# Kernel tuning notes

Hardware: AMD Instinct MI355X
Metric: run time of the kernel (lower is better)

## Reference

```python
import jax, jax.numpy as jnp
import numpy as np
from jax import lax

B, S, PH, N = 4, 512, 4096, 16384
D, G, H, L, FF, GS = 1024, 128, 8, 4, 4096, 32
HD = D // H


def setup_inputs() -> dict:
    key = jax.random.key(0)
    ks = list(jax.random.split(key, 16))
    r = lambda k, sh: jax.random.normal(k, sh, jnp.float32) * 0.02
    return {
        'last_hidden': jax.random.normal(ks[0], (B, S, PH), jnp.float32),
        'current_pointcloud': jax.random.normal(ks[1], (B, N, 3), jnp.float32),
        'fp_w': r(ks[2], (D, PH)), 'fp_b': jnp.zeros((D,), jnp.float32),
        'sp_w': r(ks[3], (G * D, D)), 'sp_b': jnp.zeros((G * D,), jnp.float32),
        'pos_embed': r(ks[4], (1, G, D)),
        'ln1_w': jnp.ones((L, D), jnp.float32), 'ln1_b': jnp.zeros((L, D), jnp.float32),
        'in_w': r(ks[5], (L, 3 * D, D)), 'in_b': jnp.zeros((L, 3 * D), jnp.float32),
        'out_w': r(ks[6], (L, D, D)), 'out_b': jnp.zeros((L, D), jnp.float32),
        'ln2_w': jnp.ones((L, D), jnp.float32), 'ln2_b': jnp.zeros((L, D), jnp.float32),
        'mlp_w1': r(ks[7], (L, FF, D)), 'mlp_b1': jnp.zeros((L, FF), jnp.float32),
        'mlp_w2': r(ks[8], (L, D, FF)), 'mlp_b2': jnp.zeros((L, D), jnp.float32),
        'c1_w': r(ks[9], (D, D)), 'c1_b': jnp.zeros((D,), jnp.float32),
        'bn_g': jnp.ones((D,), jnp.float32), 'bn_beta': jnp.zeros((D,), jnp.float32),
        'bn_m': jnp.zeros((D,), jnp.float32), 'bn_v': jnp.ones((D,), jnp.float32),
        'c2_w': r(ks[10], (3 * GS, D)), 'c2_b': jnp.zeros((3 * GS,), jnp.float32),
    }


def _ln(x, w, b):
    m = jnp.mean(x, -1, keepdims=True)
    v = jnp.mean(jnp.square(x - m), -1, keepdims=True)
    return (x - m) * lax.rsqrt(v + 1e-5) * w + b


def _fps(xyz, num_samples):
    # iterative farthest point sampling; deterministic start index 0
    Bb, Nn, _ = xyz.shape
    dist0 = jnp.full((Bb, Nn), 1e10, xyz.dtype)
    far0 = jnp.zeros((Bb,), jnp.int32)

    def step(carry, _):
        dist, far = carry
        centroid = jnp.take_along_axis(xyz, far[:, None, None], axis=1)  # [B,1,3]
        d = jnp.sum(jnp.square(xyz - centroid), -1)                      # [B,N]
        dist = jnp.minimum(dist, d)
        return (dist, jnp.argmax(dist, -1).astype(jnp.int32)), far

    _, cents = lax.scan(step, (dist0, far0), None, length=num_samples)
    cents = cents.T  # [B, num_samples]
    return jnp.take_along_axis(xyz, cents[:, :, None], axis=1)  # [B,num_samples,3]


def reference(last_hidden, current_pointcloud, fp_w, fp_b, sp_w, sp_b, pos_embed,
              ln1_w, ln1_b, in_w, in_b, out_w, out_b, ln2_w, ln2_b,
              mlp_w1, mlp_b1, mlp_w2, mlp_b2,
              c1_w, c1_b, bn_g, bn_beta, bn_m, bn_v, c2_w, c2_b):
    bsz = last_hidden.shape[0]
    agg = jnp.mean(last_hidden @ fp_w.T + fp_b, axis=1)          # [B,D]
    x = (agg @ sp_w.T + sp_b).reshape(bsz, G, D)                 # [B,G,D]
    centers = _fps(current_pointcloud, G)                        # [B,G,3]
    scale = 1.0 / np.sqrt(HD).astype(np.float32)

    def block(x, p):
        l1w, l1b, iw, ib, ow, ob, l2w, l2b, w1, b1, w2, b2 = p
        xn = _ln(x + pos_embed, l1w, l1b)
        qkv = xn @ iw.T + ib                                     # [B,G,3D]
        q, k, v = jnp.split(qkv, 3, axis=-1)
        hsp = lambda t: t.reshape(bsz, G, H, HD).transpose(0, 2, 1, 3)
        q, k, v = hsp(q), hsp(k), hsp(v)
        a = jax.nn.softmax(jnp.einsum('bhqd,bhkd->bhqk', q, k) * scale, axis=-1)
        o = jnp.einsum('bhqk,bhkd->bhqd', a, v).transpose(0, 2, 1, 3).reshape(bsz, G, D)
        x = x + o @ ow.T + ob
        h = jax.nn.gelu(_ln(x, l2w, l2b) @ w1.T + b1, approximate=False)
        return x + h @ w2.T + b2, None

    x, _ = lax.scan(block, x, (ln1_w, ln1_b, in_w, in_b, out_w, out_b,
                               ln2_w, ln2_b, mlp_w1, mlp_b1, mlp_w2, mlp_b2))

    # future_predictor: 1x1 conv == per-token linear; BN in eval mode
    h = x @ c1_w.T + c1_b
    h = jax.nn.relu((h - bn_m) * lax.rsqrt(bn_v + 1e-5) * bn_g + bn_beta)
    deltas = (h @ c2_w.T + c2_b).reshape(bsz * G, GS, 3)
    pred = deltas + centers.reshape(bsz * G, 1, 3)
    return pred.reshape(bsz, G * GS, 3)
```

## Files before the change

kernel.cpp:

```cpp
#include <hip/hip_runtime.h>
#include <hip/hip_bf16.h>
#include <math.h>


typedef __bf16 bf16x8_t __attribute__((ext_vector_type(8)));
typedef float  f32x4_t  __attribute__((ext_vector_type(4)));

__device__ __forceinline__ float wredsum(float v){
#pragma unroll
  for (int o = 32; o; o >>= 1) v += __shfl_down(v, o, 64);
  return v;
}

__device__ __forceinline__ bf16x8_t pack8(float4 a, float4 b){
  bf16x8_t v;
  v[0]=(__bf16)a.x; v[1]=(__bf16)a.y; v[2]=(__bf16)a.z; v[3]=(__bf16)a.w;
  v[4]=(__bf16)b.x; v[5]=(__bf16)b.y; v[6]=(__bf16)b.z; v[7]=(__bf16)b.w;
  return v;
}

__device__ __forceinline__ void gload16(const void* g, void* l){
  __builtin_amdgcn_global_load_lds((const __attribute__((address_space(1))) unsigned int*)g,
                                   (__attribute__((address_space(3))) unsigned int*)l, 16, 0, 0);
}

__global__ __launch_bounds__(1024) void fused_front(
  const float* __restrict__ pc, float* __restrict__ centers,
  const float* __restrict__ agg, const float* __restrict__ spw,
  const float* __restrict__ spb, float* __restrict__ x,
  const float* __restrict__ inw, const float* __restrict__ outw,
  const float* __restrict__ w1, const float* __restrict__ w2,
  const float* __restrict__ c1w, __bf16* __restrict__ wbf)
{
  const int bid = blockIdx.x;
  const int tid = threadIdx.x;
  if (bid < 4){
    const int b = bid;
    const int lane = tid & 63;
    const float* base = pc + (size_t)b * 16384 * 3;
    float px[16], py[16], pz[16], dist[16];
    {
      union { float4 v4[12]; float f[48]; } u;
      const float4* src = (const float4*)(base + tid * 48);
#pragma unroll
      for (int q = 0; q < 12; ++q) u.v4[q] = src[q];
#pragma unroll
      for (int j = 0; j < 16; ++j){
        px[j] = u.f[j*3]; py[j] = u.f[j*3+1]; pz[j] = u.f[j*3+2];
        dist[j] = 1e10f;
      }
    }
    __shared__ unsigned long long keyslot[128];
    for (int i = tid; i < 128; i += 1024) keyslot[i] = 0ULL;
    __syncthreads();
    float cx = base[0], cy = base[1], cz = base[2];
    for (int t = 0; t < 128; ++t){
      if (tid == 0){
        centers[(b*128+t)*3+0] = cx;
        centers[(b*128+t)*3+1] = cy;
        centers[(b*128+t)*3+2] = cz;
      }
      if (t == 127) break;
      float bmax = -1.0f; int bidx = 0;
#pragma unroll
      for (int j = 0; j < 16; ++j){
        float dx = __fsub_rn(px[j], cx);
        float dy = __fsub_rn(py[j], cy);
        float dz = __fsub_rn(pz[j], cz);
        float d  = __fadd_rn(__fadd_rn(__fmul_rn(dx,dx), __fmul_rn(dy,dy)), __fmul_rn(dz,dz));
        float nd = fminf(dist[j], d);
        dist[j] = nd;
        if (nd > bmax){ bmax = nd; bidx = tid*16 + j; }
      }
      unsigned long long key = ((unsigned long long)__float_as_uint(bmax) << 32)
                             | (unsigned long long)(0xFFFFFFFFu - (unsigned)bidx);
#pragma unroll
      for (int o = 32; o; o >>= 1){
        unsigned long long ok = __shfl_down(key, o, 64);
        if (ok > key) key = ok;
      }
      if (lane == 0) atomicMax(&keyslot[t], key);
      __syncthreads();
      const unsigned long long gk = keyslot[t];
      const unsigned gidx = 0xFFFFFFFFu - (unsigned)(gk & 0xFFFFFFFFu);
      const float* cp = base + (size_t)gidx*3;
      cx = cp[0]; cy = cp[1]; cz = cp[2];
    }
  } else if (bid < 1028){
    __shared__ float ag[4096];
    for (int i = tid; i < 4096; i += 1024) ag[i] = agg[i];
    __syncthreads();
    const int wv = tid >> 6, lane = tid & 63;
    const int rbase = ((bid - 4)*16 + wv)*8;
    for (int rr = 0; rr < 8; ++rr){
      const int row = rbase + rr;
      const float* wp = spw + (size_t)row*1024 + lane*4;
      const float4 w0 = *(const float4*)(wp      );
      const float4 wq1 = *(const float4*)(wp + 256);
      const float4 wq2 = *(const float4*)(wp + 512);
      const float4 wq3 = *(const float4*)(wp + 768);
      float acc[4];
#pragma unroll
      for (int bb = 0; bb < 4; ++bb){
        const float* gp = &ag[bb*1024 + lane*4];
        const float4 g0 = *(const float4*)(gp      );
        const float4 g1 = *(const float4*)(gp + 256);
        const float4 g2 = *(const float4*)(gp + 512);
        const float4 g3 = *(const float4*)(gp + 768);
        acc[bb] = w0.x*g0.x + w0.y*g0.y + w0.z*g0.z + w0.w*g0.w
                + wq1.x*g1.x + wq1.y*g1.y + wq1.z*g1.z + wq1.w*g1.w
                + wq2.x*g2.x + wq2.y*g2.y + wq2.z*g2.z + wq2.w*g2.w
                + wq3.x*g3.x + wq3.y*g3.y + wq3.z*g3.z + wq3.w*g3.w;
      }
      float a0 = wredsum(acc[0]);
      float a1 = wredsum(acc[1]);
      float a2 = wredsum(acc[2]);
      float a3 = wredsum(acc[3]);
      if (lane == 0){
        const float bias = spb[row];
        x[(size_t)0*131072 + row] = a0 + bias;
        x[(size_t)1*131072 + row] = a1 + bias;
        x[(size_t)2*131072 + row] = a2 + bias;
        x[(size_t)3*131072 + row] = a3 + bias;
      }
    }
  } else {
    const size_t t = (size_t)(bid - 1028)*1024 + tid;
    const size_t i = t*8;
    const float* src;
    if (i < 50331648){
      const size_t l = i / 12582912, r = i - l*12582912;
      if (r < 3145728)       src = inw  + l*3145728 + r;
      else if (r < 4194304)  src = outw + l*1048576 + (r-3145728);
      else if (r < 8388608)  src = w1   + l*4194304 + (r-4194304);
      else                   src = w2   + l*4194304 + (r-8388608);
    } else src = c1w + (i - 50331648);
    float4 a = *(const float4*)src, bq = *(const float4*)(src+4);
    *(bf16x8_t*)(wbf + i) = pack8(a, bq);
  }
}

__global__ __launch_bounds__(256) void partial_kernel(const float* __restrict__ lh,
                                                      float* __restrict__ part){
  const int ph = blockIdx.x*256 + threadIdx.x;
  const int sc = blockIdx.y, b = blockIdx.z;
  const float* p = lh + ((size_t)b*512 + sc*64)*4096 + ph;
  float s0=0,s1=0,s2=0,s3=0;
  for (int j = 0; j < 64; j += 4){
    s0 += p[(size_t)(j+0)*4096];
    s1 += p[(size_t)(j+1)*4096];
    s2 += p[(size_t)(j+2)*4096];
    s3 += p[(size_t)(j+3)*4096];
  }
  part[(size_t)(b*8+sc)*4096 + ph] = (s0+s1)+(s2+s3);
}

__global__ __launch_bounds__(256) void combine_kernel(const float* __restrict__ part,
                                                      float* __restrict__ mlh){
  const int i = blockIdx.x*256 + threadIdx.x;
  const int b = i >> 12, ph = i & 4095;
  float s = 0;
#pragma unroll
  for (int sc = 0; sc < 8; ++sc) s += part[(size_t)(b*8+sc)*4096 + ph];
  mlh[i] = s * (1.0f/512.0f);
}

__global__ __launch_bounds__(256) void agg_kernel(const float* __restrict__ mlh,
                                                  const float* __restrict__ fpw,
                                                  const float* __restrict__ fpb,
                                                  float* __restrict__ agg){
  const int o = blockIdx.x*4 + (threadIdx.x>>6);
  const int lane = threadIdx.x & 63;
  const int b = o >> 10, d = o & 1023;
  const float* mp = mlh + b*4096;
  const float* wp = fpw + (size_t)d*4096;
  float s = 0;
#pragma unroll 4
  for (int j = 0; j < 64; ++j){
    int ph = lane + j*64;
    s += mp[ph] * wp[ph];
  }
  s = wredsum(s);
  if (lane == 0) agg[o] = s + fpb[d];
}

__global__ __launch_bounds__(256) void ln_kernel(const float* __restrict__ x,
                                                 const float* __restrict__ pos,
                                                 const float* __restrict__ w,
                                                 const float* __restrict__ bb,
                                                 __bf16* __restrict__ out){
  const int tok = blockIdx.x, g = tok & 127, t = threadIdx.x;
  const int lane = t & 63, wv = t >> 6;
  const float* xr = x + (size_t)tok*1024;
  float v[4];
#pragma unroll
  for (int j = 0; j < 4; ++j){
    int d = t + j*256;
    float val = xr[d];
    if (pos) val += pos[g*1024 + d];
    v[j] = val;
  }
  __shared__ float r1[4], r2[4];
  float s = wredsum(v[0]+v[1]+v[2]+v[3]);
  if (lane == 0) r1[wv] = s;
  __syncthreads();
  const float mean = (r1[0]+r1[1]+r1[2]+r1[3]) * (1.0f/1024.0f);
  float sq = 0;
#pragma unroll
  for (int j = 0; j < 4; ++j){ float d0 = v[j]-mean; sq += d0*d0; }
  sq = wredsum(sq);
  if (lane == 0) r2[wv] = sq;
  __syncthreads();
  const float var = (r2[0]+r2[1]+r2[2]+r2[3]) * (1.0f/1024.0f);
  const float rs = rsqrtf(var + 1e-5f);
#pragma unroll
  for (int j = 0; j < 4; ++j){
    int d = t + j*256;
    out[(size_t)tok*1024 + d] = (__bf16)((v[j]-mean)*rs*w[d] + bb[d]);
  }
}

__global__ __launch_bounds__(256) void gemm_sk(
  const __bf16* __restrict__ A, const __bf16* __restrict__ W,
  float* __restrict__ parts, int M, int N, int K, int kc)
{
  __shared__ __bf16 As[128*32];
  __shared__ __bf16 Ws[128*32];
  const int n0 = blockIdx.x*128, m0 = blockIdx.y*128, z = blockIdx.z;
  const int tid = threadIdx.x;
  const int lane = tid & 63, w = tid >> 6;
  const int wm = w >> 1, wn = w & 1;
  const int lr = lane & 15, g = lane >> 4;
  const int kbeg = z*kc, kend = kbeg + kc;
  f32x4_t acc[4][4] = {};
  for (int k0 = kbeg; k0 < kend; k0 += 32){
    __syncthreads();
#pragma unroll
    for (int i = 0; i < 2; ++i){
      const int c = tid + i*256;
      const int row = c >> 2, q = c & 3;
      gload16(A + (size_t)(m0+row)*K + k0 + q*8, &As[(size_t)c*8]);
      gload16(W + (size_t)(n0+row)*K + k0 + q*8, &Ws[(size_t)c*8]);
    }
    __syncthreads();
    bf16x8_t af[4], bf[4];
#pragma unroll
    for (int f = 0; f < 4; ++f){
      af[f] = *(bf16x8_t*)&As[(wm*64 + f*16 + lr)*32 + g*8];
      bf[f] = *(bf16x8_t*)&Ws[(wn*64 + f*16 + lr)*32 + g*8];
    }
#pragma unroll
    for (int i = 0; i < 4; ++i)
#pragma unroll
      for (int j = 0; j < 4; ++j)
        acc[i][j] = __builtin_amdgcn_mfma_f32_16x16x32_bf16(af[i], bf[j], acc[i][j], 0, 0, 0);
  }
  float* C = parts + (size_t)z*M*N;
#pragma unroll
  for (int i = 0; i < 4; ++i)
#pragma unroll
    for (int j = 0; j < 4; ++j)
#pragma unroll
      for (int r = 0; r < 4; ++r){
        const int row = m0 + wm*64 + i*16 + g*4 + r;
        const int col = n0 + wn*64 + j*16 + lr;
        C[(size_t)row*N + col] = acc[i][j][r];
      }
}

__global__ __launch_bounds__(256) void comb_qkv(const float* __restrict__ parts,
                                                const float* __restrict__ bias,
                                                __bf16* __restrict__ out){
  const int i = blockIdx.x*256 + threadIdx.x;
  const int col = i % 3072;
  float s = 0;
#pragma unroll
  for (int z = 0; z < 4; ++z) s += parts[(size_t)z*1572864 + i];
  out[i] = (__bf16)(s + bias[col]);
}

__global__ __launch_bounds__(256) void comb_gelu(const float* __restrict__ parts,
                                                 const float* __restrict__ bias,
                                                 __bf16* __restrict__ out){
  const int i = blockIdx.x*256 + threadIdx.x;
  const int col = i & 4095;
  float v = 0;
#pragma unroll
  for (int z = 0; z < 4; ++z) v += parts[(size_t)z*2097152 + i];
  v += bias[col];
  v = v * 0.5f * (1.0f + erff(v * 0.70710678118654752440f));
  out[i] = (__bf16)v;
}

template<int MODE>
__global__ __launch_bounds__(256) void comb_res_ln(const float* __restrict__ parts, int nsplit,
                                                   const float* __restrict__ bias,
                                                   const float* __restrict__ pos,
                                                   const float* __restrict__ lw,
                                                   const float* __restrict__ lb,
                                                   float* __restrict__ x,
                                                   __bf16* __restrict__ xn){
  const int tok = blockIdx.x, gi = tok & 127, t = threadIdx.x;
  const int lane = t & 63, wv = t >> 6;
  float v[4];
#pragma unroll
  for (int j = 0; j < 4; ++j){
    const int d = t + j*256;
    const size_t idx = (size_t)tok*1024 + d;
    float s = 0;
    for (int z = 0; z < nsplit; ++z) s += parts[(size_t)z*524288 + idx];
    float val = x[idx] + s + bias[d];
    x[idx] = val;
    v[j] = val;
  }
  if (MODE == 2){
#pragma unroll
    for (int j = 0; j < 4; ++j){
      const int d = t + j*256;
      xn[(size_t)tok*1024 + d] = (__bf16)v[j];
    }
    return;
  }
  float u[4];
#pragma unroll
  for (int j = 0; j < 4; ++j){
    const int d = t + j*256;
    u[j] = v[j] + (MODE == 1 ? pos[gi*1024 + d] : 0.0f);
  }
  __shared__ float r1[4], r2[4];
  float s1 = wredsum(u[0]+u[1]+u[2]+u[3]);
  if (lane == 0) r1[wv] = s1;
  __syncthreads();
  const float mean = (r1[0]+r1[1]+r1[2]+r1[3]) * (1.0f/1024.0f);
  float sq = 0;
#pragma unroll
  for (int j = 0; j < 4; ++j){ float d0 = u[j]-mean; sq += d0*d0; }
  sq = wredsum(sq);
  if (lane == 0) r2[wv] = sq;
  __syncthreads();
  const float var = (r2[0]+r2[1]+r2[2]+r2[3]) * (1.0f/1024.0f);
  const float rs = rsqrtf(var + 1e-5f);
#pragma unroll
  for (int j = 0; j < 4; ++j){
    const int d = t + j*256;
    xn[(size_t)tok*1024 + d] = (__bf16)((u[j]-mean)*rs*lw[d] + lb[d]);
  }
}

__global__ __launch_bounds__(256) void comb_bn(const float* __restrict__ parts, int nsplit,
                                               const float* __restrict__ bias,
                                               const float* __restrict__ bnm,
                                               const float* __restrict__ bnv,
                                               const float* __restrict__ bng,
                                               const float* __restrict__ bnb,
                                               float* __restrict__ out){
  const int i = blockIdx.x*256 + threadIdx.x;
  const int c = i & 1023;
  float s = 0;
  for (int z = 0; z < nsplit; ++z) s += parts[(size_t)z*524288 + i];
  float v = s + bias[c];
  v = (v - bnm[c]) * rsqrtf(bnv[c] + 1e-5f) * bng[c] + bnb[c];
  out[i] = fmaxf(v, 0.0f);
}

__global__ __launch_bounds__(256) void attn_fused(const __bf16* __restrict__ qkv,
                                                  __bf16* __restrict__ O){
  const int bh = blockIdx.x >> 1, half = blockIdx.x & 1;
  const int b = bh>>3, h = bh&7;
  const int tid = threadIdx.x, w = tid>>6, lane = tid&63;
  const int lr = lane&15, g = lane>>4;
  __shared__ __bf16 vt[128*128];
  __shared__ __bf16 pl[4*2048];
  {
    const int n = tid >> 1, kh = tid & 1;
    const __bf16* vbase = qkv + (size_t)(b*128)*3072 + 2048 + h*128 + n;
#pragma unroll
    for (int jb = 0; jb < 8; ++jb){
      bf16x8_t pk;
#pragma unroll
      for (int e = 0; e < 8; ++e) pk[e] = vbase[(size_t)(kh*64 + jb*8 + e)*3072];
      const int cb = kh*8 + jb;
      *(bf16x8_t*)&vt[n*128 + ((cb ^ (n&7)) * 8)] = pk;
    }
  }
  const __bf16* qbase = qkv + (size_t)(b*128)*3072 + h*128;
  const __bf16* kbase = qbase + 1024;
  const int qrow0 = half*64 + w*16;
  f32x4_t acc[8] = {};
#pragma unroll
  for (int ks = 0; ks < 4; ++ks){
    bf16x8_t aq, bk[8];
    aq = *(const bf16x8_t*)(qbase + (size_t)(qrow0 + lr)*3072 + ks*32 + g*8);
#pragma unroll
    for (int j = 0; j < 8; ++j)
      bk[j] = *(const bf16x8_t*)(kbase + (size_t)(j*16 + lr)*3072 + ks*32 + g*8);
#pragma unroll
    for (int j = 0; j < 8; ++j)
      acc[j] = __builtin_amdgcn_mfma_f32_16x16x32_bf16(aq, bk[j], acc[j], 0, 0, 0);
  }
  __syncthreads();
  const float scale = 0.088388347648318447f;
#pragma unroll
  for (int r = 0; r < 4; ++r){
    const int row = g*4 + r;
    float sv[8];
    float mx = -1e30f;
#pragma unroll
    for (int j = 0; j < 8; ++j){ sv[j] = acc[j][r]*scale; mx = fmaxf(mx, sv[j]); }
#pragma unroll
    for (int o = 1; o < 16; o <<= 1) mx = fmaxf(mx, __shfl_xor(mx, o, 64));
    float s = 0;
#pragma unroll
    for (int j = 0; j < 8; ++j){ sv[j] = expf(sv[j]-mx); s += sv[j]; }
#pragma unroll
    for (int o = 1; o < 16; o <<= 1) s += __shfl_xor(s, o, 64);
    const float inv = 1.0f/s;
#pragma unroll
    for (int j = 0; j < 8; ++j){
      const int col = j*16 + lr;
      const int slot = (col>>3) ^ (row&7);
      pl[w*2048 + row*128 + slot*8 + (lr&7)] = (__bf16)(sv[j]*inv);
    }
  }
  __syncthreads();
  f32x4_t acc2[8] = {};
#pragma unroll
  for (int ks = 0; ks < 4; ++ks){
    bf16x8_t ap, bv[8];
    {
      const int row = lr;
      const int slot = (ks*4 + g) ^ (row&7);
      ap = *(bf16x8_t*)&pl[w*2048 + row*128 + slot*8];
    }
#pragma unroll
    for (int j = 0; j < 8; ++j){
      const int rowv = j*16 + lr;
      const int cb = ks*4 + g;
      bv[j] = *(bf16x8_t*)&vt[rowv*128 + ((cb ^ (rowv&7))*8)];
    }
#pragma unroll
    for (int j = 0; j < 8; ++j)
      acc2[j] = __builtin_amdgcn_mfma_f32_16x16x32_bf16(ap, bv[j], acc2[j], 0, 0, 0);
  }
#pragma unroll
  for (int j = 0; j < 8; ++j)
#pragma unroll
    for (int r = 0; r < 4; ++r){
      const int row = qrow0 + g*4 + r;
      const int col = j*16 + lr;
      O[(size_t)(b*128+row)*1024 + h*128 + col] = (__bf16)acc2[j][r];
    }
}

__global__ __launch_bounds__(256) void c2_kernel(const float* __restrict__ hb,
                                                 const float* __restrict__ w,
                                                 const float* __restrict__ bb,
                                                 const float* __restrict__ centers,
                                                 float* __restrict__ out){
  const int o = blockIdx.x*4 + (threadIdx.x>>6);
  const int lane = threadIdx.x & 63;
  const int tok = o / 96, n = o % 96;
  const float* hp = hb + (size_t)tok*1024;
  const float* wp = w + (size_t)n*1024;
  float s = 0;
#pragma unroll 4
  for (int j = 0; j < 16; ++j){
    int k = lane + j*64;
    s += hp[k] * wp[k];
  }
  s = wredsum(s);
  if (lane == 0) out[o] = s + bb[n] + centers[tok*3 + (n % 3)];
}

extern "C" void kernel_launch(void* const* d_in, const int* in_sizes, int n_in,
                              void* d_out, int out_size, void* d_ws, size_t ws_size,
                              hipStream_t stream){
  const float* lh   = (const float*)d_in[0];
  const float* pc   = (const float*)d_in[1];
  const float* fpw  = (const float*)d_in[2];
  const float* fpb  = (const float*)d_in[3];
  const float* spw  = (const float*)d_in[4];
  const float* spb  = (const float*)d_in[5];
  const float* pos  = (const float*)d_in[6];
  const float* ln1w = (const float*)d_in[7];
  const float* ln1b = (const float*)d_in[8];
  const float* inw  = (const float*)d_in[9];
  const float* inb  = (const float*)d_in[10];
  const float* outw = (const float*)d_in[11];
  const float* outb = (const float*)d_in[12];
  const float* ln2w = (const float*)d_in[13];
  const float* ln2b = (const float*)d_in[14];
  const float* w1   = (const float*)d_in[15];
  const float* b1   = (const float*)d_in[16];
  const float* w2   = (const float*)d_in[17];
  const float* b2   = (const float*)d_in[18];
  const float* c1w  = (const float*)d_in[19];
  const float* c1b  = (const float*)d_in[20];
  const float* bng  = (const float*)d_in[21];
  const float* bnbt = (const float*)d_in[22];
  const float* bnm  = (const float*)d_in[23];
  const float* bnv  = (const float*)d_in[24];
  const float* c2w  = (const float*)d_in[25];
  const float* c2b  = (const float*)d_in[26];
  float* out = (float*)d_out;

  float* f = (float*)d_ws;
  float* parts = f;              f += 16*524288;
  float* part  = f;              f += 131072;
  float* mlh   = f;              f += 16384;
  float* agg   = f;              f += 4096;
  float* x     = f;              f += 524288;
  float* hc1   = f;              f += 524288;
  float* cent  = f;              f += 2048;
  __bf16* bfp = (__bf16*)f;
  __bf16* xn   = bfp;            bfp += 524288;
  __bf16* qkv  = bfp;            bfp += 1572864;
  __bf16* obuf = bfp;            bfp += 524288;
  __bf16* hbf  = bfp;            bfp += 2097152;
  __bf16* xbf  = bfp;            bfp += 524288;
  __bf16* wbf  = bfp;            bfp += 51380224;

  partial_kernel<<<dim3(16,8,4), 256, 0, stream>>>(lh, part);
  combine_kernel<<<64, 256, 0, stream>>>(part, mlh);
  agg_kernel<<<1024, 256, 0, stream>>>(mlh, fpw, fpb, agg);
  fused_front<<<7300, 1024, 0, stream>>>(pc, cent, agg, spw, spb, x,
                                         inw, outw, w1, w2, c1w, wbf);
  ln_kernel<<<512, 256, 0, stream>>>(x, pos, ln1w, ln1b, xn);

  for (int l = 0; l < 4; ++l){
    const __bf16* wl = wbf + (size_t)l*12582912;
    gemm_sk<<<dim3(24,4,4), 256, 0, stream>>>(xn, wl, parts, 512, 3072, 1024, 256);
    comb_qkv<<<6144, 256, 0, stream>>>(parts, inb + l*3072, qkv);
    attn_fused<<<64, 256, 0, stream>>>(qkv, obuf);
    gemm_sk<<<dim3(8,4,8), 256, 0, stream>>>(obuf, wl + 3145728, parts, 512, 1024, 1024, 128);
    comb_res_ln<0><<<512, 256, 0, stream>>>(parts, 8, outb + l*1024, nullptr,
                                            ln2w + l*1024, ln2b + l*1024, x, xn);
    gemm_sk<<<dim3(32,4,4), 256, 0, stream>>>(xn, wl + 4194304, parts, 512, 4096, 1024, 256);
    comb_gelu<<<8192, 256, 0, stream>>>(parts, b1 + l*4096, hbf);
    gemm_sk<<<dim3(8,4,16), 256, 0, stream>>>(hbf, wl + 8388608, parts, 512, 1024, 4096, 256);
    if (l < 3)
      comb_res_ln<1><<<512, 256, 0, stream>>>(parts, 16, b2 + l*1024, pos,
                                              ln1w + (l+1)*1024, ln1b + (l+1)*1024, x, xn);
    else
      comb_res_ln<2><<<512, 256, 0, stream>>>(parts, 16, b2 + l*1024, nullptr,
                                              nullptr, nullptr, x, xbf);
  }

  gemm_sk<<<dim3(8,4,8), 256, 0, stream>>>(xbf, wbf + 50331648, parts, 512, 1024, 1024, 128);
  comb_bn<<<2048, 256, 0, stream>>>(parts, 8, c1b, bnm, bnv, bng, bnbt, hc1);
  c2_kernel<<<12288, 256, 0, stream>>>(hc1, c2w, c2b, cent, out);
}
```

Measured before the change: 805.4 us.

## Replace split-K GEMMs and combine kernels with full-K GEMMs and fused epilogues

Drops split-K partial-sum buffers and the separate combine kernels (bias, GELU, residual, batch-norm). Each GEMM now runs over the full K with 512-thread blocks and applies its epilogue directly, and LayerNorm moves back to a standalone ln_kernel. This removes the traffic of writing and re-reading the fp32 partial sums and cuts the number of launches. In exchange the grids shrink sharply (for example 32 blocks for the N=1024 GEMMs) and each block runs a long single-buffered K loop, so the device may be badly underused. ln_kernel is also now called with a null pos pointer, which relies on it handling that case.

```diff
diff --git a/kernel.cpp b/kernel.cpp
--- a/kernel.cpp
+++ b/kernel.cpp
@@ -220,147 +220,68 @@
   }
 }
 
-__global__ __launch_bounds__(256) void gemm_sk(
+template<int EPI>
+__global__ __launch_bounds__(512) void gemm_full(
   const __bf16* __restrict__ A, const __bf16* __restrict__ W,
-  float* __restrict__ parts, int M, int N, int K, int kc)
+  const float* __restrict__ bias, void* __restrict__ Cv,
+  int M, int N, int K,
+  float* __restrict__ xres, __bf16* __restrict__ xbcopy,
+  const float* __restrict__ bnm, const float* __restrict__ bnv,
+  const float* __restrict__ bng, const float* __restrict__ bnb)
 {
   __shared__ __bf16 As[128*32];
   __shared__ __bf16 Ws[128*32];
-  const int n0 = blockIdx.x*128, m0 = blockIdx.y*128, z = blockIdx.z;
+  const int n0 = blockIdx.x*128, m0 = blockIdx.y*128;
   const int tid = threadIdx.x;
   const int lane = tid & 63, w = tid >> 6;
   const int wm = w >> 1, wn = w & 1;
   const int lr = lane & 15, g = lane >> 4;
-  const int kbeg = z*kc, kend = kbeg + kc;
-  f32x4_t acc[4][4] = {};
-  for (int k0 = kbeg; k0 < kend; k0 += 32){
+  const int crow = tid >> 2, cq = tid & 3;
+  const __bf16* ap = A + (size_t)(m0 + crow)*K + cq*8;
+  const __bf16* wp = W + (size_t)(n0 + crow)*K + cq*8;
+  f32x4_t acc[2][4] = {};
+  for (int k0 = 0; k0 < K; k0 += 32){
     __syncthreads();
-#pragma unroll
-    for (int i = 0; i < 2; ++i){
-      const int c = tid + i*256;
-      const int row = c >> 2, q = c & 3;
-      gload16(A + (size_t)(m0+row)*K + k0 + q*8, &As[(size_t)c*8]);
-      gload16(W + (size_t)(n0+row)*K + k0 + q*8, &Ws[(size_t)c*8]);
-    }
+    gload16(ap + k0, &As[(size_t)tid*8]);
+    gload16(wp + k0, &Ws[(size_t)tid*8]);
     __syncthreads();
-    bf16x8_t af[4], bf[4];
-#pragma unroll
-    for (int f = 0; f < 4; ++f){
-      af[f] = *(bf16x8_t*)&As[(wm*64 + f*16 + lr)*32 + g*8];
-      bf[f] = *(bf16x8_t*)&Ws[(wn*64 + f*16 + lr)*32 + g*8];
-    }
-#pragma unroll
-    for (int i = 0; i < 4; ++i)
+    bf16x8_t af[2], bf[4];
+#pragma unroll
+    for (int i = 0; i < 2; ++i)
+      af[i] = *(bf16x8_t*)&As[(wm*32 + i*16 + lr)*32 + g*8];
+#pragma unroll
+    for (int j = 0; j < 4; ++j)
+      bf[j] = *(bf16x8_t*)&Ws[(wn*64 + j*16 + lr)*32 + g*8];
+#pragma unroll
+    for (int i = 0; i < 2; ++i)
 #pragma unroll
       for (int j = 0; j < 4; ++j)
         acc[i][j] = __builtin_amdgcn_mfma_f32_16x16x32_bf16(af[i], bf[j], acc[i][j], 0, 0, 0);
   }
-  float* C = parts + (size_t)z*M*N;
-#pragma unroll
-  for (int i = 0; i < 4; ++i)
+#pragma unroll
+  for (int i = 0; i < 2; ++i)
 #pragma unroll
     for (int j = 0; j < 4; ++j)
 #pragma unroll
       for (int r = 0; r < 4; ++r){
-        const int row = m0 + wm*64 + i*16 + g*4 + r;
+        const int row = m0 + wm*32 + i*16 + g*4 + r;
         const int col = n0 + wn*64 + j*16 + lr;
-        C[(size_t)row*N + col] = acc[i][j][r];
-      }
-}
-
-__global__ __launch_bounds__(256) void comb_qkv(const float* __restrict__ parts,
-                                                const float* __restrict__ bias,
-                                                __bf16* __restrict__ out){
-  const int i = blockIdx.x*256 + threadIdx.x;
-  const int col = i % 3072;
-  float s = 0;
-#pragma unroll
-  for (int z = 0; z < 4; ++z) s += parts[(size_t)z*1572864 + i];
-  out[i] = (__bf16)(s + bias[col]);
-}
-
-__global__ __launch_bounds__(256) void comb_gelu(const float* __restrict__ parts,
-                                                 const float* __restrict__ bias,
-                                                 __bf16* __restrict__ out){
-  const int i = blockIdx.x*256 + threadIdx.x;
-  const int col = i & 4095;
-  float v = 0;
-#pragma unroll
-  for (int z = 0; z < 4; ++z) v += parts[(size_t)z*2097152 + i];
-  v += bias[col];
-  v = v * 0.5f * (1.0f + erff(v * 0.70710678118654752440f));
-  out[i] = (__bf16)v;
-}
-
-template<int MODE>
-__global__ __launch_bounds__(256) void comb_res_ln(const float* __restrict__ parts, int nsplit,
-                                                   const float* __restrict__ bias,
-                                                   const float* __restrict__ pos,
-                                                   const float* __restrict__ lw,
-                                                   const float* __restrict__ lb,
-                                                   float* __restrict__ x,
-                                                   __bf16* __restrict__ xn){
-  const int tok = blockIdx.x, gi = tok & 127, t = threadIdx.x;
-  const int lane = t & 63, wv = t >> 6;
-  float v[4];
-#pragma unroll
-  for (int j = 0; j < 4; ++j){
-    const int d = t + j*256;
-    const size_t idx = (size_t)tok*1024 + d;
-    float s = 0;
-    for (int z = 0; z < nsplit; ++z) s += parts[(size_t)z*524288 + idx];
-    float val = x[idx] + s + bias[d];
-    x[idx] = val;
-    v[j] = val;
-  }
-  if (MODE == 2){
-#pragma unroll
-    for (int j = 0; j < 4; ++j){
-      const int d = t + j*256;
-      xn[(size_t)tok*1024 + d] = (__bf16)v[j];
-    }
-    return;
-  }
-  float u[4];
-#pragma unroll
-  for (int j = 0; j < 4; ++j){
-    const int d = t + j*256;
-    u[j] = v[j] + (MODE == 1 ? pos[gi*1024 + d] : 0.0f);
-  }
-  __shared__ float r1[4], r2[4];
-  float s1 = wredsum(u[0]+u[1]+u[2]+u[3]);
-  if (lane == 0) r1[wv] = s1;
-  __syncthreads();
-  const float mean = (r1[0]+r1[1]+r1[2]+r1[3]) * (1.0f/1024.0f);
-  float sq = 0;
-#pragma unroll
-  for (int j = 0; j < 4; ++j){ float d0 = u[j]-mean; sq += d0*d0; }
-  sq = wredsum(sq);
-  if (lane == 0) r2[wv] = sq;
-  __syncthreads();
-  const float var = (r2[0]+r2[1]+r2[2]+r2[3]) * (1.0f/1024.0f);
-  const float rs = rsqrtf(var + 1e-5f);
-#pragma unroll
-  for (int j = 0; j < 4; ++j){
-    const int d = t + j*256;
-    xn[(size_t)tok*1024 + d] = (__bf16)((u[j]-mean)*rs*lw[d] + lb[d]);
-  }
-}
-
-__global__ __launch_bounds__(256) void comb_bn(const float* __restrict__ parts, int nsplit,
-                                               const float* __restrict__ bias,
-                                               const float* __restrict__ bnm,
-                                               const float* __restrict__ bnv,
-                                               const float* __restrict__ bng,
-                                               const float* __restrict__ bnb,
-                                               float* __restrict__ out){
-  const int i = blockIdx.x*256 + threadIdx.x;
-  const int c = i & 1023;
-  float s = 0;
-  for (int z = 0; z < nsplit; ++z) s += parts[(size_t)z*524288 + i];
-  float v = s + bias[c];
-  v = (v - bnm[c]) * rsqrtf(bnv[c] + 1e-5f) * bng[c] + bnb[c];
-  out[i] = fmaxf(v, 0.0f);
+        const size_t idx = (size_t)row*N + col;
+        float v = acc[i][j][r] + bias[col];
+        if (EPI == 0){
+          ((__bf16*)Cv)[idx] = (__bf16)v;
+        } else if (EPI == 1){
+          v += xres[idx];
+          ((float*)Cv)[idx] = v;
+          if (xbcopy) xbcopy[idx] = (__bf16)v;
+        } else if (EPI == 2){
+          v = v * 0.5f * (1.0f + erff(v * 0.70710678118654752440f));
+          ((__bf16*)Cv)[idx] = (__bf16)v;
+        } else {
+          v = (v - bnm[col]) * rsqrtf(bnv[col] + 1e-5f) * bng[col] + bnb[col];
+          ((float*)Cv)[idx] = fmaxf(v, 0.0f);
+        }
+      }
 }
 
 __global__ __launch_bounds__(256) void attn_fused(const __bf16* __restrict__ qkv,
@@ -505,7 +426,6 @@
   float* out = (float*)d_out;
 
   float* f = (float*)d_ws;
-  float* parts = f;              f += 16*524288;
   float* part  = f;              f += 131072;
   float* mlh   = f;              f += 16384;
   float* agg   = f;              f += 4096;
@@ -529,24 +449,26 @@
 
   for (int l = 0; l < 4; ++l){
     const __bf16* wl = wbf + (size_t)l*12582912;
-    gemm_sk<<<dim3(24,4,4), 256, 0, stream>>>(xn, wl, parts, 512, 3072, 1024, 256);
-    comb_qkv<<<6144, 256, 0, stream>>>(parts, inb + l*3072, qkv);
+    gemm_full<0><<<dim3(24,4), 512, 0, stream>>>(xn, wl, inb + l*3072, qkv,
+                                                 512, 3072, 1024,
+                                                 nullptr, nullptr, nullptr, nullptr, nullptr, nullptr);
     attn_fused<<<64, 256, 0, stream>>>(qkv, obuf);
-    gemm_sk<<<dim3(8,4,8), 256, 0, stream>>>(obuf, wl + 3145728, parts, 512, 1024, 1024, 128);
-    comb_res_ln<0><<<512, 256, 0, stream>>>(parts, 8, outb + l*1024, nullptr,
-                                            ln2w + l*1024, ln2b + l*1024, x, xn);
-    gemm_sk<<<dim3(32,4,4), 256, 0, stream>>>(xn, wl + 4194304, parts, 512, 4096, 1024, 256);
-    comb_gelu<<<8192, 256, 0, stream>>>(parts, b1 + l*4096, hbf);
-    gemm_sk<<<dim3(8,4,16), 256, 0, stream>>>(hbf, wl + 8388608, parts, 512, 1024, 4096, 256);
+    gemm_full<1><<<dim3(8,4), 512, 0, stream>>>(obuf, wl + 3145728, outb + l*1024, x,
+                                                512, 1024, 1024,
+                                                x, nullptr, nullptr, nullptr, nullptr, nullptr);
+    ln_kernel<<<512, 256, 0, stream>>>(x, nullptr, ln2w + l*1024, ln2b + l*1024, xn);
+    gemm_full<2><<<dim3(32,4), 512, 0, stream>>>(xn, wl + 4194304, b1 + l*4096, hbf,
+                                                 512, 4096, 1024,
+                                                 nullptr, nullptr, nullptr, nullptr, nullptr, nullptr);
+    gemm_full<1><<<dim3(8,4), 512, 0, stream>>>(hbf, wl + 8388608, b2 + l*1024, x,
+                                                512, 1024, 4096,
+                                                x, (l==3) ? xbf : nullptr, nullptr, nullptr, nullptr, nullptr);
     if (l < 3)
-      comb_res_ln<1><<<512, 256, 0, stream>>>(parts, 16, b2 + l*1024, pos,
-                                              ln1w + (l+1)*1024, ln1b + (l+1)*1024, x, xn);
-    else
-      comb_res_ln<2><<<512, 256, 0, stream>>>(parts, 16, b2 + l*1024, nullptr,
-                                              nullptr, nullptr, x, xbf);
-  }
-
-  gemm_sk<<<dim3(8,4,8), 256, 0, stream>>>(xbf, wbf + 50331648, parts, 512, 1024, 1024, 128);
-  comb_bn<<<2048, 256, 0, stream>>>(parts, 8, c1b, bnm, bnv, bng, bnbt, hc1);
+      ln_kernel<<<512, 256, 0, stream>>>(x, pos, ln1w + (l+1)*1024, ln1b + (l+1)*1024, xn);
+  }
+
+  gemm_full<3><<<dim3(8,4), 512, 0, stream>>>(xbf, wbf + 50331648, c1b, hc1,
+                                              512, 1024, 1024,
+                                              nullptr, nullptr, bnm, bnv, bng, bnbt);
   c2_kernel<<<12288, 256, 0, stream>>>(hc1, c2w, c2b, cent, out);
 }
```

New measurement: 1.070 ms. 1.33x slower.

## Fuse QKV split-K combine into attention, halve split-K, fuse head kernels

Applied to the files above, without the earlier changes.

Removes the comb_qkv kernel: the attention kernel now sums the two split-K partials plus bias while loading Q, K and V, so the bf16 qkv buffer is no longer materialised. Split-K factors for the QKV, MLP1 and MLP2 GEMMs are halved to cut partial-sum traffic and combine work. The combine GEMM also gains a larger per-split K chunk. The BN combine and c2 projection are merged into one per-token head kernel that keeps the activation row in shared memory. Attention now reads fp32 partials with redundant per-block reads, and fewer GEMM blocks may reduce occupancy.

```diff
diff --git a/kernel.cpp b/kernel.cpp
--- a/kernel.cpp
+++ b/kernel.cpp
@@ -268,26 +268,12 @@
       }
 }
 
-__global__ __launch_bounds__(256) void comb_qkv(const float* __restrict__ parts,
-                                                const float* __restrict__ bias,
-                                                __bf16* __restrict__ out){
-  const int i = blockIdx.x*256 + threadIdx.x;
-  const int col = i % 3072;
-  float s = 0;
-#pragma unroll
-  for (int z = 0; z < 4; ++z) s += parts[(size_t)z*1572864 + i];
-  out[i] = (__bf16)(s + bias[col]);
-}
-
 __global__ __launch_bounds__(256) void comb_gelu(const float* __restrict__ parts,
                                                  const float* __restrict__ bias,
                                                  __bf16* __restrict__ out){
   const int i = blockIdx.x*256 + threadIdx.x;
   const int col = i & 4095;
-  float v = 0;
-#pragma unroll
-  for (int z = 0; z < 4; ++z) v += parts[(size_t)z*2097152 + i];
-  v += bias[col];
+  float v = parts[i] + parts[2097152 + i] + bias[col];
   v = v * 0.5f * (1.0f + erff(v * 0.70710678118654752440f));
   out[i] = (__bf16)v;
 }
@@ -347,23 +333,9 @@
   }
 }
 
-__global__ __launch_bounds__(256) void comb_bn(const float* __restrict__ parts, int nsplit,
-                                               const float* __restrict__ bias,
-                                               const float* __restrict__ bnm,
-                                               const float* __restrict__ bnv,
-                                               const float* __restrict__ bng,
-                                               const float* __restrict__ bnb,
-                                               float* __restrict__ out){
-  const int i = blockIdx.x*256 + threadIdx.x;
-  const int c = i & 1023;
-  float s = 0;
-  for (int z = 0; z < nsplit; ++z) s += parts[(size_t)z*524288 + i];
-  float v = s + bias[c];
-  v = (v - bnm[c]) * rsqrtf(bnv[c] + 1e-5f) * bng[c] + bnb[c];
-  out[i] = fmaxf(v, 0.0f);
-}
-
-__global__ __launch_bounds__(256) void attn_fused(const __bf16* __restrict__ qkv,
+__global__ __launch_bounds__(256) void attn_fused(const float* __restrict__ p0,
+                                                  const float* __restrict__ p1,
+                                                  const float* __restrict__ bias,
                                                   __bf16* __restrict__ O){
   const int bh = blockIdx.x >> 1, half = blockIdx.x & 1;
   const int b = bh>>3, h = bh&7;
@@ -373,27 +345,48 @@
   __shared__ __bf16 pl[4*2048];
   {
     const int n = tid >> 1, kh = tid & 1;
-    const __bf16* vbase = qkv + (size_t)(b*128)*3072 + 2048 + h*128 + n;
+    const size_t vb0 = (size_t)(b*128)*3072 + 2048 + h*128 + n;
+    const float vbias = bias[2048 + h*128 + n];
 #pragma unroll
     for (int jb = 0; jb < 8; ++jb){
       bf16x8_t pk;
 #pragma unroll
-      for (int e = 0; e < 8; ++e) pk[e] = vbase[(size_t)(kh*64 + jb*8 + e)*3072];
+      for (int e = 0; e < 8; ++e){
+        const size_t off = vb0 + (size_t)(kh*64 + jb*8 + e)*3072;
+        pk[e] = (__bf16)(p0[off] + p1[off] + vbias);
+      }
       const int cb = kh*8 + jb;
       *(bf16x8_t*)&vt[n*128 + ((cb ^ (n&7)) * 8)] = pk;
     }
   }
-  const __bf16* qbase = qkv + (size_t)(b*128)*3072 + h*128;
-  const __bf16* kbase = qbase + 1024;
   const int qrow0 = half*64 + w*16;
   f32x4_t acc[8] = {};
 #pragma unroll
   for (int ks = 0; ks < 4; ++ks){
     bf16x8_t aq, bk[8];
-    aq = *(const bf16x8_t*)(qbase + (size_t)(qrow0 + lr)*3072 + ks*32 + g*8);
-#pragma unroll
-    for (int j = 0; j < 8; ++j)
-      bk[j] = *(const bf16x8_t*)(kbase + (size_t)(j*16 + lr)*3072 + ks*32 + g*8);
+    {
+      const int cq = h*128 + ks*32 + g*8;
+      const size_t idx = (size_t)(b*128 + qrow0 + lr)*3072 + cq;
+      const float4 a0 = *(const float4*)(p0+idx), a1 = *(const float4*)(p0+idx+4);
+      const float4 b0 = *(const float4*)(p1+idx), b1 = *(const float4*)(p1+idx+4);
+      const float4 c0 = *(const float4*)(bias+cq), c1 = *(const float4*)(bias+cq+4);
+      float4 lo, hi;
+      lo.x=a0.x+b0.x+c0.x; lo.y=a0.y+b0.y+c0.y; lo.z=a0.z+b0.z+c0.z; lo.w=a0.w+b0.w+c0.w;
+      hi.x=a1.x+b1.x+c1.x; hi.y=a1.y+b1.y+c1.y; hi.z=a1.z+b1.z+c1.z; hi.w=a1.w+b1.w+c1.w;
+      aq = pack8(lo, hi);
+    }
+#pragma unroll
+    for (int j = 0; j < 8; ++j){
+      const int ck = 1024 + h*128 + ks*32 + g*8;
+      const size_t idx = (size_t)(b*128 + j*16 + lr)*3072 + ck;
+      const float4 a0 = *(const float4*)(p0+idx), a1 = *(const float4*)(p0+idx+4);
+      const float4 b0 = *(const float4*)(p1+idx), b1 = *(const float4*)(p1+idx+4);
+      const float4 c0 = *(const float4*)(bias+ck), c1 = *(const float4*)(bias+ck+4);
+      float4 lo, hi;
+      lo.x=a0.x+b0.x+c0.x; lo.y=a0.y+b0.y+c0.y; lo.z=a0.z+b0.z+c0.z; lo.w=a0.w+b0.w+c0.w;
+      hi.x=a1.x+b1.x+c1.x; hi.y=a1.y+b1.y+c1.y; hi.z=a1.z+b1.z+c1.z; hi.w=a1.w+b1.w+c1.w;
+      bk[j] = pack8(lo, hi);
+    }
 #pragma unroll
     for (int j = 0; j < 8; ++j)
       acc[j] = __builtin_amdgcn_mfma_f32_16x16x32_bf16(aq, bk[j], acc[j], 0, 0, 0);
@@ -452,24 +445,43 @@
     }
 }
 
-__global__ __launch_bounds__(256) void c2_kernel(const float* __restrict__ hb,
-                                                 const float* __restrict__ w,
-                                                 const float* __restrict__ bb,
-                                                 const float* __restrict__ centers,
-                                                 float* __restrict__ out){
-  const int o = blockIdx.x*4 + (threadIdx.x>>6);
-  const int lane = threadIdx.x & 63;
-  const int tok = o / 96, n = o % 96;
-  const float* hp = hb + (size_t)tok*1024;
-  const float* wp = w + (size_t)n*1024;
-  float s = 0;
+__global__ __launch_bounds__(256) void head_kernel(const float* __restrict__ parts,
+                                                   const float* __restrict__ c1b,
+                                                   const float* __restrict__ bnm,
+                                                   const float* __restrict__ bnv,
+                                                   const float* __restrict__ bng,
+                                                   const float* __restrict__ bnb,
+                                                   const float* __restrict__ c2w,
+                                                   const float* __restrict__ c2b,
+                                                   const float* __restrict__ centers,
+                                                   float* __restrict__ out){
+  const int tok = blockIdx.x, t = threadIdx.x;
+  const int wv = t >> 6, lane = t & 63;
+  __shared__ float hrow[1024];
+#pragma unroll
+  for (int j = 0; j < 4; ++j){
+    const int d = t + j*256;
+    const size_t idx = (size_t)tok*1024 + d;
+    float s = 0;
+#pragma unroll
+    for (int z = 0; z < 8; ++z) s += parts[(size_t)z*524288 + idx];
+    float v = s + c1b[d];
+    v = (v - bnm[d]) * rsqrtf(bnv[d] + 1e-5f) * bng[d] + bnb[d];
+    hrow[d] = fmaxf(v, 0.0f);
+  }
+  __syncthreads();
+  for (int i = 0; i < 24; ++i){
+    const int n = wv*24 + i;
+    const float* wp = c2w + (size_t)n*1024;
+    float s = 0;
 #pragma unroll 4
-  for (int j = 0; j < 16; ++j){
-    int k = lane + j*64;
-    s += hp[k] * wp[k];
-  }
-  s = wredsum(s);
-  if (lane == 0) out[o] = s + bb[n] + centers[tok*3 + (n % 3)];
+    for (int j = 0; j < 16; ++j){
+      const int k = lane + j*64;
+      s += hrow[k] * wp[k];
+    }
+    s = wredsum(s);
+    if (lane == 0) out[(size_t)tok*96 + n] = s + c2b[n] + centers[tok*3 + (n % 3)];
+  }
 }
 
 extern "C" void kernel_launch(void* const* d_in, const int* in_sizes, int n_in,
@@ -510,11 +522,9 @@
   float* mlh   = f;              f += 16384;
   float* agg   = f;              f += 4096;
   float* x     = f;              f += 524288;
-  float* hc1   = f;              f += 524288;
   float* cent  = f;              f += 2048;
   __bf16* bfp = (__bf16*)f;
   __bf16* xn   = bfp;            bfp += 524288;
-  __bf16* qkv  = bfp;            bfp += 1572864;
   __bf16* obuf = bfp;            bfp += 524288;
   __bf16* hbf  = bfp;            bfp += 2097152;
   __bf16* xbf  = bfp;            bfp += 524288;
@@ -529,24 +539,22 @@
 
   for (int l = 0; l < 4; ++l){
     const __bf16* wl = wbf + (size_t)l*12582912;
-    gemm_sk<<<dim3(24,4,4), 256, 0, stream>>>(xn, wl, parts, 512, 3072, 1024, 256);
-    comb_qkv<<<6144, 256, 0, stream>>>(parts, inb + l*3072, qkv);
-    attn_fused<<<64, 256, 0, stream>>>(qkv, obuf);
+    gemm_sk<<<dim3(24,4,2), 256, 0, stream>>>(xn, wl, parts, 512, 3072, 1024, 512);
+    attn_fused<<<64, 256, 0, stream>>>(parts, parts + 1572864, inb + l*3072, obuf);
     gemm_sk<<<dim3(8,4,8), 256, 0, stream>>>(obuf, wl + 3145728, parts, 512, 1024, 1024, 128);
     comb_res_ln<0><<<512, 256, 0, stream>>>(parts, 8, outb + l*1024, nullptr,
                                             ln2w + l*1024, ln2b + l*1024, x, xn);
-    gemm_sk<<<dim3(32,4,4), 256, 0, stream>>>(xn, wl + 4194304, parts, 512, 4096, 1024, 256);
+    gemm_sk<<<dim3(32,4,2), 256, 0, stream>>>(xn, wl + 4194304, parts, 512, 4096, 1024, 512);
     comb_gelu<<<8192, 256, 0, stream>>>(parts, b1 + l*4096, hbf);
-    gemm_sk<<<dim3(8,4,16), 256, 0, stream>>>(hbf, wl + 8388608, parts, 512, 1024, 4096, 256);
+    gemm_sk<<<dim3(8,4,8), 256, 0, stream>>>(hbf, wl + 8388608, parts, 512, 1024, 4096, 512);
     if (l < 3)
-      comb_res_ln<1><<<512, 256, 0, stream>>>(parts, 16, b2 + l*1024, pos,
+      comb_res_ln<1><<<512, 256, 0, stream>>>(parts, 8, b2 + l*1024, pos,
                                               ln1w + (l+1)*1024, ln1b + (l+1)*1024, x, xn);
     else
-      comb_res_ln<2><<<512, 256, 0, stream>>>(parts, 16, b2 + l*1024, nullptr,
+      comb_res_ln<2><<<512, 256, 0, stream>>>(parts, 8, b2 + l*1024, nullptr,
                                               nullptr, nullptr, x, xbf);
   }
 
   gemm_sk<<<dim3(8,4,8), 256, 0, stream>>>(xbf, wbf + 50331648, parts, 512, 1024, 1024, 128);
-  comb_bn<<<2048, 256, 0, stream>>>(parts, 8, c1b, bnm, bnv, bng, bnbt, hc1);
-  c2_kernel<<<12288, 256, 0, stream>>>(hc1, c2w, c2b, cent, out);
-}
+  head_kernel<<<512, 256, 0, stream>>>(parts, c1b, bnm, bnv, bng, bnbt, c2w, c2b, cent, out);
+}
```

Measured after the change: 872.5 us. 8.3% more time.
